# Optimization experiments

Hardware: AMD Instinct MI355X
Metric: run time of the kernel (lower is better)

The kernel has to match this reference:

```python
import jax, jax.numpy as jnp
import numpy as np

K = 16  # neighbors (module's self.k)


def _gather(points, idx):
    # points (B,C,N), idx (B,M[,k]) -> (B,C,M[,k])
    return jax.vmap(lambda p, i: p[:, i])(points, idx)


def _fps(xyz, nsample):
    # furthest point sampling on xyz (B,3,N) -> idx (B,nsample) int32
    B, _, N = xyz.shape

    def body(carry, _):
        dists, last = carry
        lp = jnp.take_along_axis(xyz, last[:, None, None], axis=2)  # (B,3,1)
        d = jnp.sum((xyz - lp) ** 2, axis=1)  # (B,N)
        dists = jnp.minimum(dists, d)
        nxt = jnp.argmax(dists, axis=1).astype(jnp.int32)
        return (dists, nxt), nxt

    init_idx = jnp.zeros((B,), dtype=jnp.int32)
    init_d = jnp.full((B, N), jnp.finfo(xyz.dtype).max, xyz.dtype)
    _, rest = jax.lax.scan(body, (init_d, init_idx), None, length=nsample - 1)
    return jnp.concatenate([init_idx[None], rest], axis=0).T  # (B,nsample)


def _knn(query, points, k):
    # query (B,C,M), points (B,C,N): k nearest in feature space
    d = (jnp.sum(query ** 2, axis=1)[:, :, None]
         + jnp.sum(points ** 2, axis=1)[:, None, :]
         - 2.0 * jnp.einsum('bcm,bcn->bmn', query, points))  # (B,M,N)
    _, idx = jax.lax.top_k(-d, k)  # (B,M,k)
    return _gather(points, idx), idx  # (B,C,M,k), (B,M,k)


def _conv1x1(W, b, y):
    # y (B,Cin,M,k), W (Cout,Cin) -> (B,Cout,M,k)
    return jnp.einsum('oi,bimk->bomk', W, y) + b[None, :, None, None]


def setup_inputs() -> dict:
    key = jax.random.key(0)
    ks = jax.random.split(key, 8)
    B, C, N = 4, 64, 8192
    g = 64
    return {
        'x': jax.random.normal(ks[0], (B, C, N), jnp.float32),
        'xyz': jax.random.normal(ks[1], (B, 3, N), jnp.float32),
        'W0': jax.random.normal(ks[2], (g, 2 * C), jnp.float32) * 0.05,
        'b0': jax.random.normal(ks[3], (g,), jnp.float32) * 0.05,
        'W1': jax.random.normal(ks[4], (g, C + g), jnp.float32) * 0.05,
        'b1': jax.random.normal(ks[5], (g,), jnp.float32) * 0.05,
        'W2': jax.random.normal(ks[6], (g, C + 2 * g), jnp.float32) * 0.05,
        'b2': jax.random.normal(ks[7], (g,), jnp.float32) * 0.05,
        'nsample': 2048,
    }


def reference(x, xyz, W0, b0, W1, b1, W2, b2, nsample):
    # furthest point sample on coordinates, gather sampled features
    sampled_idx = _fps(xyz, nsample)              # (B,M)
    sampled_xyz = _gather(xyz, sampled_idx)       # (B,3,M)
    sampled_x = _gather(x, sampled_idx)           # (B,C,M)
    # local graph: k+1 NN in feature space, drop self
    knn_pt, _ = _knn(sampled_x, x, K + 1)
    knn_pt = knn_pt[..., 1:]                      # (B,C,M,K)
    center = sampled_x[..., None]                 # (B,C,M,1)
    center_k = jnp.broadcast_to(center, knn_pt.shape)
    edge = jnp.concatenate([center_k, knn_pt - center_k], axis=1)  # (B,2C,M,K)
    # dense edge conv cascade
    y = jnp.concatenate([jax.nn.relu(_conv1x1(W0, b0, edge)), center_k], axis=1)
    y = jnp.concatenate([jax.nn.relu(_conv1x1(W1, b1, y)), y], axis=1)
    y = jnp.concatenate([_conv1x1(W2, b2, y), y], axis=1)
    y = jnp.max(y, axis=-1)                       # (B, C+3*g, M)
    return (y, sampled_xyz, sampled_idx)
```

## Files before the change

kernel.cpp:

```cpp
#include <hip/hip_runtime.h>
#include <hip/hip_bf16.h>
#include <stdint.h>

typedef unsigned long long u64;
typedef unsigned int u32;
typedef unsigned short u16;

#define B_   4
#define C_   64
#define N_   8192
#define M_   2048
#define KNB  16
#define FLT_MAX_ 3.402823466e+38f

__device__ __forceinline__ int clampN(int v) {
    return v < 0 ? 0 : (v > N_ - 1 ? N_ - 1 : v);
}


__device__ __forceinline__ void pin4(float4& v) {
    asm volatile("" : "+v"(v.x), "+v"(v.y), "+v"(v.z), "+v"(v.w));
}

__device__ __forceinline__ float wave_fmax_dpp(float v) {
    float t;
    t = __int_as_float(__builtin_amdgcn_update_dpp(0, __float_as_int(v), 0x111, 0xf, 0xf, true)); v = fmaxf(v, t);
    t = __int_as_float(__builtin_amdgcn_update_dpp(0, __float_as_int(v), 0x112, 0xf, 0xf, true)); v = fmaxf(v, t);
    t = __int_as_float(__builtin_amdgcn_update_dpp(0, __float_as_int(v), 0x114, 0xf, 0xf, true)); v = fmaxf(v, t);
    t = __int_as_float(__builtin_amdgcn_update_dpp(0, __float_as_int(v), 0x118, 0xf, 0xf, true)); v = fmaxf(v, t);
    t = __int_as_float(__builtin_amdgcn_update_dpp(0, __float_as_int(v), 0x142, 0xa, 0xf, true)); v = fmaxf(v, t);
    t = __int_as_float(__builtin_amdgcn_update_dpp(0, __float_as_int(v), 0x143, 0xc, 0xf, true)); v = fmaxf(v, t);
    return __int_as_float(__builtin_amdgcn_readlane(__float_as_int(v), 63));
}

#define FPS_STEP(PX, PY, PZ, DD, J)                                          \
    {                                                                        \
        float dx = __fsub_rn((PX), lx);                                      \
        float dy = __fsub_rn((PY), ly);                                      \
        float dz = __fsub_rn((PZ), lz);                                      \
        float d = __fadd_rn(__fadd_rn(__fmul_rn(dx, dx), __fmul_rn(dy, dy)), \
                            __fmul_rn(dz, dz));                              \
        float nd = fminf((DD), d);                                           \
        (DD) = nd;                                                           \
        bool gt = nd > fm;                                                   \
        fm = gt ? nd : fm;                                                   \
        fj = gt ? (J) : fj;                                                  \
        fx = gt ? (PX) : fx;                                                 \
        fy = gt ? (PY) : fy;                                                 \
        fz = gt ? (PZ) : fz;                                                 \
    }

__global__ __launch_bounds__(512, 2) void fps_kernel(const float* __restrict__ xyz,
                                                     u16* __restrict__ idx_ws) {
    const int b = blockIdx.x & 3;
    const int tid = threadIdx.x;
    const int lane = tid & 63;
    const int w = tid >> 6;
    const float* xb = xyz + b * 3 * N_;
    const int n0 = tid * 16;

    float4 px[4], py[4], pz[4], dd[4];
#pragma unroll
    for (int j4 = 0; j4 < 4; ++j4) {
        px[j4] = *(const float4*)(xb + n0 + j4 * 4);
        py[j4] = *(const float4*)(xb + N_ + n0 + j4 * 4);
        pz[j4] = *(const float4*)(xb + 2 * N_ + n0 + j4 * 4);
        pin4(px[j4]); pin4(py[j4]); pin4(pz[j4]);
        dd[j4] = make_float4(FLT_MAX_, FLT_MAX_, FLT_MAX_, FLT_MAX_);
    }

    __shared__ float4 red4[2][8];
    __shared__ int    redi[2][8];

    int cur = 0;
    float lx = xb[0], ly = xb[N_], lz = xb[2 * N_];
    if (tid == 0) idx_ws[b * M_ + 0] = 0;

    for (int s = 1; s < M_; ++s) {
        float fm = -1.0f, fx = 0.f, fy = 0.f, fz = 0.f;
        int fj = 0;
#pragma unroll
        for (int j4 = 0; j4 < 4; ++j4) {
            FPS_STEP(px[j4].x, py[j4].x, pz[j4].x, dd[j4].x, j4 * 4 + 0);
            FPS_STEP(px[j4].y, py[j4].y, pz[j4].y, dd[j4].y, j4 * 4 + 1);
            FPS_STEP(px[j4].z, py[j4].z, pz[j4].z, dd[j4].z, j4 * 4 + 2);
            FPS_STEP(px[j4].w, py[j4].w, pz[j4].w, dd[j4].w, j4 * 4 + 3);
        }
        float wm = wave_fmax_dpp(fm);
        u64 bal = __ballot(fm == wm);
        int winlane = (int)__ffsll(bal) - 1;
        const int par = s & 1;
        if (lane == winlane) {
            red4[par][w] = make_float4(wm, fx, fy, fz);
            redi[par][w] = n0 + fj;
        }
        __syncthreads();
        float4 p0 = red4[par][0];
        float g = p0.x; float nlx = p0.y, nly = p0.z, nlz = p0.w;
        int ncur = redi[par][0];
#pragma unroll
        for (int ww = 1; ww < 8; ++ww) {
            float4 p = red4[par][ww];
            int id = redi[par][ww];
            bool gt = p.x > g;
            g = gt ? p.x : g;
            nlx = gt ? p.y : nlx; nly = gt ? p.z : nly; nlz = gt ? p.w : nlz;
            ncur = gt ? id : ncur;
        }
        lx = nlx; ly = nly; lz = nlz; cur = ncur;
        if (tid == 0) idx_ws[b * M_ + s] = (u16)cur;
    }
}

__global__ __launch_bounds__(256) void gather_kernel(const float* __restrict__ xyz,
                                                     const u16* __restrict__ idx_ws,
                                                     float* __restrict__ out1,
                                                     float* __restrict__ out2) {
    int gid = blockIdx.x * 256 + threadIdx.x;
    int b = gid >> 11, m = gid & 2047;
    int idx = clampN((int)idx_ws[b * M_ + m]);
    out2[b * M_ + m] = (float)idx;
    const float* xyzb = xyz + b * 3 * N_;
#pragma unroll
    for (int d = 0; d < 3; ++d)
        out1[(b * 3 + d) * M_ + m] = xyzb[d * N_ + idx];
}

__global__ __launch_bounds__(256) void pnorm_kernel(const float* __restrict__ x,
                                                    float* __restrict__ pnorm_ws) {
    int gid = blockIdx.x * 256 + threadIdx.x;
    int b = gid >> 13, n = gid & 8191;
    const float* xb = x + b * C_ * N_ + n;
    float acc = 0.f;
#pragma unroll 16
    for (int c = 0; c < C_; ++c) { float v = xb[c * N_]; acc = fmaf(v, v, acc); }
    pnorm_ws[gid] = acc;
}

__global__ __launch_bounds__(256) void wtrans_kernel(const float* __restrict__ W0,
                                                     const float* __restrict__ W1,
                                                     const float* __restrict__ W2,
                                                     float* __restrict__ wt) {
    int e = blockIdx.x * 256 + threadIdx.x;
    if (e < 8192) {
        int i = e >> 6, o = e & 63;
        wt[e] = W0[o * 128 + i];
    } else if (e < 16384) {
        int e2 = e - 8192; int i = e2 >> 6, o = e2 & 63;
        wt[8192 + e2] = W1[o * 128 + i];
    } else {
        int e2 = e - 16384; int i = e2 >> 6, o = e2 & 63;
        wt[16384 + e2] = W2[o * 192 + i];
    }
}

__global__ __launch_bounds__(256) void knn_kernel(const float* __restrict__ x,
                                                  const u16* __restrict__ idx_ws,
                                                  const float* __restrict__ pnorm_ws,
                                                  u16* __restrict__ nbr_ws) {
    __shared__ float pt[64 * 68];
    __shared__ float spn[64];
    __shared__ u64 lists[256 * 17];

    const int tid = threadIdx.x;
    const int b = blockIdx.x >> 6;
    const int m0 = (blockIdx.x & 63) * 32;
    const int q = tid & 31, sub = tid >> 5;
    const int m = m0 + q;
    const float* xb = x + b * C_ * N_;
    const int self = clampN((int)idx_ws[b * M_ + m]);

    float4 qv[16];
#pragma unroll
    for (int c4 = 0; c4 < 16; ++c4) {
        qv[c4].x = xb[(c4 * 4 + 0) * N_ + self];
        qv[c4].y = xb[(c4 * 4 + 1) * N_ + self];
        qv[c4].z = xb[(c4 * 4 + 2) * N_ + self];
        qv[c4].w = xb[(c4 * 4 + 3) * N_ + self];
    }
    const float qn = pnorm_ws[b * N_ + self];

    u64* L = lists + tid * 17;
#pragma unroll
    for (int j = 0; j < 17; ++j) L[j] = ~0ULL;
    u64 worst = ~0ULL;

    for (int t = 0; t < N_ / 64; ++t) {
        const int nb0 = t * 64;
        __syncthreads();
#pragma unroll
        for (int r = 0; r < 4; ++r) {
            int e = tid + r * 256;
            int c = e >> 4, nq = e & 15;
            float4 v = *(const float4*)(xb + c * N_ + nb0 + nq * 4);
            const int cs = c ^ (nq << 2);
            pt[(nq * 4 + 0) * 68 + cs] = v.x;
            pt[(nq * 4 + 1) * 68 + cs] = v.y;
            pt[(nq * 4 + 2) * 68 + cs] = v.z;
            pt[(nq * 4 + 3) * 68 + cs] = v.w;
        }
        if (tid < 64) spn[tid] = pnorm_ws[b * N_ + nb0 + tid];
        __syncthreads();
#pragma unroll
        for (int pp = 0; pp < 8; ++pp) {
            int nl = sub * 8 + pp;
            const float* pvbase = pt + nl * 68;
            const int rsw = (nl >> 2) << 2;
            float a0 = 0.f, a1 = 0.f, a2 = 0.f, a3 = 0.f;
#pragma unroll
            for (int c4 = 0; c4 < 16; ++c4) {
                float4 p = *(const float4*)(pvbase + (((c4 << 2) ^ rsw)));
                a0 = fmaf(qv[c4].x, p.x, a0);
                a1 = fmaf(qv[c4].y, p.y, a1);
                a2 = fmaf(qv[c4].z, p.z, a2);
                a3 = fmaf(qv[c4].w, p.w, a3);
            }
            float dot = (a0 + a1) + (a2 + a3);
            float d = qn + spn[nl] - 2.0f * dot;
            u32 db = __float_as_uint(d);
            db = (db & 0x80000000u) ? ~db : (db | 0x80000000u);
            u64 key = ((u64)db << 32) | (u32)(nb0 + nl);
            if (key < worst) {
                int j = 16;
                while (j > 0 && L[j - 1] > key) { L[j] = L[j - 1]; --j; }
                L[j] = key;
                worst = L[16];
            }
        }
    }
    __syncthreads();
    if (tid < 32) {
        int pos[8];
#pragma unroll
        for (int s2 = 0; s2 < 8; ++s2) pos[s2] = 0;
        u16* outp = nbr_ws + (b * M_ + m0 + tid) * KNB;
        for (int r = 0; r < 17; ++r) {
            u64 best = ~0ULL; int bs = 0;
#pragma unroll
            for (int s2 = 0; s2 < 8; ++s2) {
                u64 k2 = (pos[s2] < 17) ? lists[(tid + 32 * s2) * 17 + pos[s2]] : ~0ULL;
                if (k2 < best) { best = k2; bs = s2; }
            }
#pragma unroll
            for (int s2 = 0; s2 < 8; ++s2) pos[s2] += (s2 == bs) ? 1 : 0;
            if (r > 0) outp[r - 1] = (u16)clampN((int)(best & 0xFFFFFFFFu));
        }
    }
}

__device__ __forceinline__ void mm_tile(float a[4][4], const float* __restrict__ w,
                                        const float* __restrict__ s, int ni) {
#pragma unroll 8
    for (int i = 0; i < ni; ++i) {
        const float4 w4 = *(const float4*)(w + i * 64);
        const float4 e4 = *(const float4*)(s + i * 64);
        a[0][0] = fmaf(w4.x, e4.x, a[0][0]);
        a[0][1] = fmaf(w4.x, e4.y, a[0][1]);
        a[0][2] = fmaf(w4.x, e4.z, a[0][2]);
        a[0][3] = fmaf(w4.x, e4.w, a[0][3]);
        a[1][0] = fmaf(w4.y, e4.x, a[1][0]);
        a[1][1] = fmaf(w4.y, e4.y, a[1][1]);
        a[1][2] = fmaf(w4.y, e4.z, a[1][2]);
        a[1][3] = fmaf(w4.y, e4.w, a[1][3]);
        a[2][0] = fmaf(w4.z, e4.x, a[2][0]);
        a[2][1] = fmaf(w4.z, e4.y, a[2][1]);
        a[2][2] = fmaf(w4.z, e4.z, a[2][2]);
        a[2][3] = fmaf(w4.z, e4.w, a[2][3]);
        a[3][0] = fmaf(w4.w, e4.x, a[3][0]);
        a[3][1] = fmaf(w4.w, e4.y, a[3][1]);
        a[3][2] = fmaf(w4.w, e4.z, a[3][2]);
        a[3][3] = fmaf(w4.w, e4.w, a[3][3]);
    }
}

__global__ __launch_bounds__(256) void conv_kernel(const float* __restrict__ x,
                                                   const u16* __restrict__ idx_ws,
                                                   const u16* __restrict__ nbr_ws,
                                                   const float* __restrict__ wt,
                                                   const float* __restrict__ bias0,
                                                   const float* __restrict__ bias1,
                                                   const float* __restrict__ bias2,
                                                   float* __restrict__ out0) {
    __shared__ float E[128 * 64];
    __shared__ float H0[64 * 64];
    __shared__ float H1[64 * 64];

    const int tid = threadIdx.x;
    const int b = blockIdx.x >> 9;
    const int m0 = (blockIdx.x & 511) * 4;
    const float* xb = x + b * C_ * N_;

    {
        const int col = tid & 63;
        const int half = tid >> 6;
        const int m = m0 + (col >> 4);
        const int k = col & 15;
        const int selfm = clampN((int)idx_ws[b * M_ + m]);
        const int nbr = clampN((int)nbr_ws[(b * M_ + m) * KNB + k]);
#pragma unroll
        for (int c2 = 0; c2 < 16; ++c2) {
            int c = half * 16 + c2;
            float ctr = xb[c * N_ + selfm];
            float nb = xb[c * N_ + nbr];
            E[c * 64 + col] = ctr;
            E[(64 + c) * 64 + col] = __fsub_rn(nb, ctr);
        }
    }
    __syncthreads();

    const int o0 = (tid >> 4) * 4;
    const int c0 = (tid & 15) * 4;
    float a[4][4];

    {
        float4 bb = *(const float4*)(bias0 + o0);
        a[0][0] = a[0][1] = a[0][2] = a[0][3] = bb.x;
        a[1][0] = a[1][1] = a[1][2] = a[1][3] = bb.y;
        a[2][0] = a[2][1] = a[2][2] = a[2][3] = bb.z;
        a[3][0] = a[3][1] = a[3][2] = a[3][3] = bb.w;
        mm_tile(a, wt + o0, E + c0, 128);
#pragma unroll
        for (int oo = 0; oo < 4; ++oo) {
            float4 v = make_float4(fmaxf(a[oo][0], 0.f), fmaxf(a[oo][1], 0.f),
                                   fmaxf(a[oo][2], 0.f), fmaxf(a[oo][3], 0.f));
            *(float4*)(H0 + (o0 + oo) * 64 + c0) = v;
        }
    }
    __syncthreads();

    {
        float4 bb = *(const float4*)(bias1 + o0);
        a[0][0] = a[0][1] = a[0][2] = a[0][3] = bb.x;
        a[1][0] = a[1][1] = a[1][2] = a[1][3] = bb.y;
        a[2][0] = a[2][1] = a[2][2] = a[2][3] = bb.z;
        a[3][0] = a[3][1] = a[3][2] = a[3][3] = bb.w;
        mm_tile(a, wt + 8192 + o0, H0 + c0, 64);
        mm_tile(a, wt + 8192 + 64 * 64 + o0, E + c0, 64);
#pragma unroll
        for (int oo = 0; oo < 4; ++oo) {
            float4 v = make_float4(fmaxf(a[oo][0], 0.f), fmaxf(a[oo][1], 0.f),
                                   fmaxf(a[oo][2], 0.f), fmaxf(a[oo][3], 0.f));
            *(float4*)(H1 + (o0 + oo) * 64 + c0) = v;
        }
    }
    __syncthreads();

    {
        float4 bb = *(const float4*)(bias2 + o0);
        a[0][0] = a[0][1] = a[0][2] = a[0][3] = bb.x;
        a[1][0] = a[1][1] = a[1][2] = a[1][3] = bb.y;
        a[2][0] = a[2][1] = a[2][2] = a[2][3] = bb.z;
        a[3][0] = a[3][1] = a[3][2] = a[3][3] = bb.w;
        mm_tile(a, wt + 16384 + o0, H1 + c0, 64);
        mm_tile(a, wt + 16384 + 64 * 64 + o0, H0 + c0, 64);
        mm_tile(a, wt + 16384 + 128 * 64 + o0, E + c0, 64);
#pragma unroll
        for (int oo = 0; oo < 4; ++oo) {
            float4 v = make_float4(a[oo][0], a[oo][1], a[oo][2], a[oo][3]);
            *(float4*)(E + (64 + o0 + oo) * 64 + c0) = v;
        }
    }
    __syncthreads();

#pragma unroll
    for (int r = 0; r < 4; ++r) {
        int e = tid + r * 256;
        int ch = e >> 2, mloc = e & 3;
        int colb = mloc * 16;
        float v;
        if (ch < 64) {
            const float* row = E + (64 + ch) * 64 + colb;
            v = row[0];
#pragma unroll
            for (int k = 1; k < 16; ++k) v = fmaxf(v, row[k]);
        } else if (ch < 128) {
            const float* row = H1 + (ch - 64) * 64 + colb;
            v = row[0];
#pragma unroll
            for (int k = 1; k < 16; ++k) v = fmaxf(v, row[k]);
        } else if (ch < 192) {
            const float* row = H0 + (ch - 128) * 64 + colb;
            v = row[0];
#pragma unroll
            for (int k = 1; k < 16; ++k) v = fmaxf(v, row[k]);
        } else {
            v = E[(ch - 192) * 64 + colb];
        }
        out0[((b * 256 + ch) << 11) + m0 + mloc] = v;
    }
}

extern "C" void kernel_launch(void* const* d_in, const int* in_sizes, int n_in,
                              void* d_out, int out_size, void* d_ws, size_t ws_size,
                              hipStream_t stream) {
    const float* x   = (const float*)d_in[0];
    const float* xyz = (const float*)d_in[1];
    const float* W0  = (const float*)d_in[2];
    const float* b0  = (const float*)d_in[3];
    const float* W1  = (const float*)d_in[4];
    const float* b1  = (const float*)d_in[5];
    const float* W2  = (const float*)d_in[6];
    const float* b2  = (const float*)d_in[7];

    float* out  = (float*)d_out;
    float* out0 = out;
    float* out1 = out + 4 * 256 * 2048;
    float* out2 = out1 + 4 * 3 * 2048;

    char* ws = (char*)d_ws;
    u16*   idx_ws   = (u16*)ws;
    u16*   nbr_ws   = (u16*)(ws + 16384);
    float* pnorm_ws = (float*)(ws + 278528);
    float* wt_ws    = (float*)(ws + 409600);

    pnorm_kernel<<<128, 256, 0, stream>>>(x, pnorm_ws);
    wtrans_kernel<<<112, 256, 0, stream>>>(W0, W1, W2, wt_ws);
    fps_kernel<<<64, 512, 0, stream>>>(xyz, idx_ws);
    gather_kernel<<<32, 256, 0, stream>>>(xyz, idx_ws, out1, out2);
    knn_kernel<<<256, 256, 0, stream>>>(x, idx_ws, pnorm_ws, nbr_ws);
    conv_kernel<<<2048, 256, 0, stream>>>(x, idx_ws, nbr_ws, wt_ws, b0, b1, b2, out0);
}
```

Measured before the change: 2.980 ms.

## Fuse FPS, gather, pnorm and weight transpose into one launch; drop H1 buffer

The pnorm, weight-transpose and gather kernels are folded into the FPS kernel. Extra blocks do the side work, and the FPS blocks keep sampled indices in shared memory and write the gathered xyz outputs themselves. This cuts three launches and lets the small prep work overlap the serial FPS loop. The conv kernel also removes its H1 shared buffer by reusing the E region and reordering the max-reduction stores, which lowers LDS use and may raise occupancy but adds one extra barrier phase.

```diff
diff --git a/kernel.cpp b/kernel.cpp
--- a/kernel.cpp
+++ b/kernel.cpp
@@ -50,10 +50,46 @@
         fz = gt ? (PZ) : fz;                                                 \
     }
 
-__global__ __launch_bounds__(512, 2) void fps_kernel(const float* __restrict__ xyz,
-                                                     u16* __restrict__ idx_ws) {
-    const int b = blockIdx.x & 3;
+__global__ __launch_bounds__(512, 2) void fps_prep_kernel(
+    const float* __restrict__ xyz, const float* __restrict__ x,
+    const float* __restrict__ W0, const float* __restrict__ W1,
+    const float* __restrict__ W2, u16* __restrict__ idx_ws,
+    float* __restrict__ pnorm_ws, float* __restrict__ wt,
+    float* __restrict__ out1, float* __restrict__ out2) {
+    const int bid = blockIdx.x;
     const int tid = threadIdx.x;
+
+    __shared__ float4 red4[2][8];
+    __shared__ int    redi[2][8];
+    __shared__ u16    hist[M_];
+
+    if (bid >= 64) {
+        if (bid < 128) {
+            int gid = (bid - 64) * 512 + tid;
+            int b = gid >> 13, n = gid & 8191;
+            const float* xb = x + b * C_ * N_ + n;
+            float acc = 0.f;
+#pragma unroll 16
+            for (int c = 0; c < C_; ++c) { float v = xb[c * N_]; acc = fmaf(v, v, acc); }
+            pnorm_ws[gid] = acc;
+        } else {
+            int e = (bid - 128) * 512 + tid;
+            if (e < 8192) {
+                int i = e >> 6, o = e & 63;
+                wt[e] = W0[o * 128 + i];
+            } else if (e < 16384) {
+                int e2 = e - 8192; int i = e2 >> 6, o = e2 & 63;
+                wt[8192 + e2] = W1[o * 128 + i];
+            } else {
+                int e2 = e - 16384; int i = e2 >> 6, o = e2 & 63;
+                wt[16384 + e2] = W2[o * 192 + i];
+            }
+        }
+        return;
+    }
+
+    const int rep = bid >> 2;
+    const int b = bid & 3;
     const int lane = tid & 63;
     const int w = tid >> 6;
     const float* xb = xyz + b * 3 * N_;
@@ -69,12 +105,9 @@
         dd[j4] = make_float4(FLT_MAX_, FLT_MAX_, FLT_MAX_, FLT_MAX_);
     }
 
-    __shared__ float4 red4[2][8];
-    __shared__ int    redi[2][8];
-
     int cur = 0;
     float lx = xb[0], ly = xb[N_], lz = xb[2 * N_];
-    if (tid == 0) idx_ws[b * M_ + 0] = 0;
+    if (tid == 0) { idx_ws[b * M_ + 0] = 0; hist[0] = 0; }
 
     for (int s = 1; s < M_; ++s) {
         float fm = -1.0f, fx = 0.f, fy = 0.f, fz = 0.f;
@@ -108,49 +141,18 @@
             ncur = gt ? id : ncur;
         }
         lx = nlx; ly = nly; lz = nlz; cur = ncur;
-        if (tid == 0) idx_ws[b * M_ + s] = (u16)cur;
-    }
-}
-
-__global__ __launch_bounds__(256) void gather_kernel(const float* __restrict__ xyz,
-                                                     const u16* __restrict__ idx_ws,
-                                                     float* __restrict__ out1,
-                                                     float* __restrict__ out2) {
-    int gid = blockIdx.x * 256 + threadIdx.x;
-    int b = gid >> 11, m = gid & 2047;
-    int idx = clampN((int)idx_ws[b * M_ + m]);
-    out2[b * M_ + m] = (float)idx;
-    const float* xyzb = xyz + b * 3 * N_;
-#pragma unroll
-    for (int d = 0; d < 3; ++d)
-        out1[(b * 3 + d) * M_ + m] = xyzb[d * N_ + idx];
-}
-
-__global__ __launch_bounds__(256) void pnorm_kernel(const float* __restrict__ x,
-                                                    float* __restrict__ pnorm_ws) {
-    int gid = blockIdx.x * 256 + threadIdx.x;
-    int b = gid >> 13, n = gid & 8191;
-    const float* xb = x + b * C_ * N_ + n;
-    float acc = 0.f;
-#pragma unroll 16
-    for (int c = 0; c < C_; ++c) { float v = xb[c * N_]; acc = fmaf(v, v, acc); }
-    pnorm_ws[gid] = acc;
-}
-
-__global__ __launch_bounds__(256) void wtrans_kernel(const float* __restrict__ W0,
-                                                     const float* __restrict__ W1,
-                                                     const float* __restrict__ W2,
-                                                     float* __restrict__ wt) {
-    int e = blockIdx.x * 256 + threadIdx.x;
-    if (e < 8192) {
-        int i = e >> 6, o = e & 63;
-        wt[e] = W0[o * 128 + i];
-    } else if (e < 16384) {
-        int e2 = e - 8192; int i = e2 >> 6, o = e2 & 63;
-        wt[8192 + e2] = W1[o * 128 + i];
-    } else {
-        int e2 = e - 16384; int i = e2 >> 6, o = e2 & 63;
-        wt[16384 + e2] = W2[o * 192 + i];
+        if (tid == 0) { idx_ws[b * M_ + s] = (u16)cur; hist[s] = (u16)cur; }
+    }
+
+    __syncthreads();
+    if (rep == 0) {
+        for (int m = tid; m < M_; m += 512) {
+            int idx = (int)hist[m];
+            out2[b * M_ + m] = (float)idx;
+            out1[(b * 3 + 0) * M_ + m] = xb[idx];
+            out1[(b * 3 + 1) * M_ + m] = xb[N_ + idx];
+            out1[(b * 3 + 2) * M_ + m] = xb[2 * N_ + idx];
+        }
     }
 }
 
@@ -283,7 +285,6 @@
                                                    float* __restrict__ out0) {
     __shared__ float E[128 * 64];
     __shared__ float H0[64 * 64];
-    __shared__ float H1[64 * 64];
 
     const int tid = threadIdx.x;
     const int b = blockIdx.x >> 9;
@@ -340,7 +341,7 @@
         for (int oo = 0; oo < 4; ++oo) {
             float4 v = make_float4(fmaxf(a[oo][0], 0.f), fmaxf(a[oo][1], 0.f),
                                    fmaxf(a[oo][2], 0.f), fmaxf(a[oo][3], 0.f));
-            *(float4*)(H1 + (o0 + oo) * 64 + c0) = v;
+            *(float4*)(E + (64 + o0 + oo) * 64 + c0) = v;
         }
     }
     __syncthreads();
@@ -351,30 +352,19 @@
         a[1][0] = a[1][1] = a[1][2] = a[1][3] = bb.y;
         a[2][0] = a[2][1] = a[2][2] = a[2][3] = bb.z;
         a[3][0] = a[3][1] = a[3][2] = a[3][3] = bb.w;
-        mm_tile(a, wt + 16384 + o0, H1 + c0, 64);
+        mm_tile(a, wt + 16384 + o0, E + 64 * 64 + c0, 64);
         mm_tile(a, wt + 16384 + 64 * 64 + o0, H0 + c0, 64);
         mm_tile(a, wt + 16384 + 128 * 64 + o0, E + c0, 64);
-#pragma unroll
-        for (int oo = 0; oo < 4; ++oo) {
-            float4 v = make_float4(a[oo][0], a[oo][1], a[oo][2], a[oo][3]);
-            *(float4*)(E + (64 + o0 + oo) * 64 + c0) = v;
-        }
-    }
-    __syncthreads();
-
-#pragma unroll
-    for (int r = 0; r < 4; ++r) {
+    }
+
+#pragma unroll
+    for (int r = 1; r < 4; ++r) {
         int e = tid + r * 256;
         int ch = e >> 2, mloc = e & 3;
         int colb = mloc * 16;
         float v;
-        if (ch < 64) {
-            const float* row = E + (64 + ch) * 64 + colb;
-            v = row[0];
-#pragma unroll
-            for (int k = 1; k < 16; ++k) v = fmaxf(v, row[k]);
-        } else if (ch < 128) {
-            const float* row = H1 + (ch - 64) * 64 + colb;
+        if (ch < 128) {
+            const float* row = E + (64 + (ch - 64)) * 64 + colb;
             v = row[0];
 #pragma unroll
             for (int k = 1; k < 16; ++k) v = fmaxf(v, row[k]);
@@ -386,6 +376,27 @@
         } else {
             v = E[(ch - 192) * 64 + colb];
         }
+        out0[((b * 256 + ch) << 11) + m0 + mloc] = v;
+    }
+    __syncthreads();
+
+    {
+#pragma unroll
+        for (int oo = 0; oo < 4; ++oo) {
+            float4 v = make_float4(a[oo][0], a[oo][1], a[oo][2], a[oo][3]);
+            *(float4*)(E + (64 + o0 + oo) * 64 + c0) = v;
+        }
+    }
+    __syncthreads();
+
+    {
+        int e = tid;
+        int ch = e >> 2, mloc = e & 3;
+        int colb = mloc * 16;
+        const float* row = E + (64 + ch) * 64 + colb;
+        float v = row[0];
+#pragma unroll
+        for (int k = 1; k < 16; ++k) v = fmaxf(v, row[k]);
         out0[((b * 256 + ch) << 11) + m0 + mloc] = v;
     }
 }
@@ -413,10 +424,8 @@
     float* pnorm_ws = (float*)(ws + 278528);
     float* wt_ws    = (float*)(ws + 409600);
 
-    pnorm_kernel<<<128, 256, 0, stream>>>(x, pnorm_ws);
-    wtrans_kernel<<<112, 256, 0, stream>>>(W0, W1, W2, wt_ws);
-    fps_kernel<<<64, 512, 0, stream>>>(xyz, idx_ws);
-    gather_kernel<<<32, 256, 0, stream>>>(xyz, idx_ws, out1, out2);
+    fps_prep_kernel<<<184, 512, 0, stream>>>(xyz, x, W0, W1, W2,
+                                             idx_ws, pnorm_ws, wt_ws, out1, out2);
     knn_kernel<<<256, 256, 0, stream>>>(x, idx_ws, pnorm_ws, nbr_ws);
     conv_kernel<<<2048, 256, 0, stream>>>(x, idx_ws, nbr_ws, wt_ws, b0, b1, b2, out0);
 }
```

Measured after the change: 2.969 ms. No clear change (-0.4%).
